# Kernel tuning notes

Hardware: AMD Instinct MI355X
Metric: run time of the kernel (lower is better)

Reference implementation:

```python
import jax, jax.numpy as jnp
import numpy as np

B, T, Hs, Ws, D, NH, NKV = 2, 8, 16, 16, 1024, 16, 4
HD = D // NH  # 64
EPS = 1e-6
THETA = 10000.0


def setup_inputs() -> dict:
    key = jax.random.key(0)
    ks = jax.random.split(key, 6)
    N = T * Hs * Ws
    s = 0.02
    return {
        'x': jax.random.normal(ks[0], (B, N, D), jnp.float32),
        'Wq': jax.random.normal(ks[1], (D, D), jnp.float32) * s,
        'bq': jnp.zeros((D,), jnp.float32),
        'Wk': jax.random.normal(ks[2], (D, NKV * HD), jnp.float32) * s,
        'bk': jnp.zeros((NKV * HD,), jnp.float32),
        'Wv': jax.random.normal(ks[3], (D, NKV * HD), jnp.float32) * s,
        'bv': jnp.zeros((NKV * HD,), jnp.float32),
        'Wo': jax.random.normal(ks[4], (D, D), jnp.float32) * s,
        'bo': jnp.zeros((D,), jnp.float32),
        'qn_w': jnp.ones((HD,), jnp.float32),
        'kn_w': jnp.ones((HD,), jnp.float32),
        't': T, 'h': Hs, 'w': Ws,
    }


def _rms_norm(x, w):
    # RMSNorm over last dim (head_dim), eps=1e-6, learned scale
    var = jnp.mean(jnp.square(x), axis=-1, keepdims=True)
    return x * jax.lax.rsqrt(var + EPS) * w


def _rope_cs(n, d):
    inv = 1.0 / (THETA ** (np.arange(0, d, 2, dtype=np.float32) / d))
    fr = np.arange(n, dtype=np.float32)[:, None] * inv[None, :]
    emb = np.concatenate([fr, fr], axis=-1)  # (n, d)
    return jnp.asarray(np.cos(emb)), jnp.asarray(np.sin(emb))


def _rot_half(x):
    x1, x2 = jnp.split(x, 2, axis=-1)
    return jnp.concatenate([-x2, x1], axis=-1)


def _st_rope(x, t, h, w):
    # x: (B, t, h, w, heads, hd); factored 3D RoPE on head_dim split
    d = x.shape[-1]
    if d % 3 == 0:
        dt = dh = d // 3
        dw = d - 2 * dt
    else:
        dt = d // 4
        dh = d // 4
        dw = d - dt - dh
    xt, xh, xw = jnp.split(x, [dt, dt + dh], axis=-1)

    def app(xs, n, axis_pos, dd):
        cos, sin = _rope_cs(n, dd)
        shp = [1] * 6
        shp[axis_pos] = n
        shp[-1] = dd
        cos = cos.reshape(shp)
        sin = sin.reshape(shp)
        return xs * cos + _rot_half(xs) * sin

    xt = app(xt, t, 1, dt)
    xh = app(xh, h, 2, dh)
    xw = app(xw, w, 3, dw)
    return jnp.concatenate([xt, xh, xw], axis=-1)


def reference(x, Wq, bq, Wk, bk, Wv, bv, Wo, bo, qn_w, kn_w, t, h, w):
    Bx, N, Dx = x.shape
    q = (x @ Wq + bq).reshape(Bx, N, NH, HD)
    k = (x @ Wk + bk).reshape(Bx, N, NKV, HD)
    v = (x @ Wv + bv).reshape(Bx, N, NKV, HD)
    q = _rms_norm(q, qn_w)
    k = _rms_norm(k, kn_w)
    q = _st_rope(q.reshape(Bx, t, h, w, NH, HD), t, h, w).reshape(Bx, N, NH, HD)
    k = _st_rope(k.reshape(Bx, t, h, w, NKV, HD), t, h, w).reshape(Bx, N, NKV, HD)
    g = NH // NKV
    if g > 1:  # GQA: 'b m h d -> b m (h g) d'
        k = jnp.repeat(k, g, axis=2)
        v = jnp.repeat(v, g, axis=2)
    scale = HD ** -0.5
    scores = jnp.einsum('bnhd,bmhd->bhnm', q, k) * scale  # (B,H,N,N)
    p = jax.nn.softmax(scores, axis=-1)
    out = jnp.einsum('bhnm,bmhd->bnhd', p, v).reshape(Bx, N, Dx)
    return out @ Wo + bo
```

## Files before the change

### kernel.cpp

```cpp
#include <hip/hip_runtime.h>
#include <hip/hip_bf16.h>
#include <math.h>

constexpr int B_   = 2;
constexpr int N_   = 2048;
constexpr int D_   = 1024;
constexpr int NH_  = 16;
constexpr int NKV_ = 4;
constexpr int HD_  = 64;
constexpr int BN_  = 4096;
constexpr int KVD_ = NKV_ * HD_;
constexpr float EPS_ = 1e-6f;
constexpr float THETA_ = 10000.0f;
constexpr float LOG2E_ = 1.4426950408889634f;

typedef _Float16 half8v __attribute__((ext_vector_type(8)));
typedef _Float16 half4v __attribute__((ext_vector_type(4)));
typedef _Float16 half2v __attribute__((ext_vector_type(2)));
typedef unsigned short ushort8v __attribute__((ext_vector_type(8)));
typedef float f32x4 __attribute__((ext_vector_type(4)));

static __device__ __forceinline__ unsigned short f2h(float f) {
  union { _Float16 h; unsigned short u; } v; v.h = (_Float16)f; return v.u;
}
static __device__ __forceinline__ float h2f(unsigned short u) {
  union { unsigned short u; _Float16 h; } v; v.u = u; return (float)v.h;
}

#if __has_builtin(__builtin_amdgcn_exp2f)
#define EXP2F(x) __builtin_amdgcn_exp2f(x)
#else
#define EXP2F(x) __expf((x) * 0.6931471805599453f)
#endif

static __device__ __forceinline__ void dma16(const unsigned short* g,
                                             unsigned short* l) {
  __builtin_amdgcn_global_load_lds(
      (const __attribute__((address_space(1))) unsigned int*)g,
      (__attribute__((address_space(3))) unsigned int*)l, 16, 0, 0);
}

static __device__ __forceinline__ void wtrans_tile(
    const float* __restrict__ W, int Nw, int K, float scale,
    unsigned short* __restrict__ WTh, unsigned short* __restrict__ WTl,
    int bx, int by, bool lo)
{
  __shared__ float tile[32][33];
  const int k0 = bx * 32, n0 = by * 32;
  const int c = threadIdx.x & 31, rb = threadIdx.x >> 5;
#pragma unroll
  for (int i = 0; i < 4; ++i) {
    const int r = rb + i * 8;
    tile[r][c] = W[(size_t)(k0 + r) * Nw + n0 + c];
  }
  __syncthreads();
#pragma unroll
  for (int i = 0; i < 4; ++i) {
    const int r = rb + i * 8;
    const float v = tile[c][r] * scale;
    const size_t o = (size_t)(n0 + r) * K + k0 + c;
    const unsigned short hi = f2h(v);
    WTh[o] = hi;
    if (lo) WTl[o] = f2h(v - h2f(hi));
  }
}

__global__ __launch_bounds__(256) void prep(
    const float* __restrict__ x,
    const float* __restrict__ Wq, const float* __restrict__ Wk,
    const float* __restrict__ Wv, const float* __restrict__ Wo,
    unsigned short* __restrict__ xh,
    unsigned short* __restrict__ WqT, unsigned short* __restrict__ WkT,
    unsigned short* __restrict__ WvT,
    unsigned short* __restrict__ WoTh, unsigned short* __restrict__ WoTl)
{
  const int bid = blockIdx.x;
  if (bid < 2048) {
    const int i = (bid * 256 + threadIdx.x) * 8;
    const float4 v0 = *(const float4*)(x + i);
    const float4 v1 = *(const float4*)(x + i + 4);
    ushort8v o;
    o[0] = f2h(v0.x); o[1] = f2h(v0.y); o[2] = f2h(v0.z); o[3] = f2h(v0.w);
    o[4] = f2h(v1.x); o[5] = f2h(v1.y); o[6] = f2h(v1.z); o[7] = f2h(v1.w);
    *(ushort8v*)(xh + i) = o;
  } else if (bid < 3072) {
    const int l = bid - 2048;
    wtrans_tile(Wq, D_, D_, 1.0f, WqT, nullptr, l & 31, l >> 5, false);
  } else if (bid < 3328) {
    const int l = bid - 3072;
    wtrans_tile(Wk, KVD_, D_, 1.0f, WkT, nullptr, l & 31, l >> 5, false);
  } else if (bid < 3584) {
    const int l = bid - 3328;
    wtrans_tile(Wv, KVD_, D_, 1.0f, WvT, nullptr, l & 31, l >> 5, false);
  } else {
    const int l = bid - 3584;
    wtrans_tile(Wo, D_, D_, 64.0f, WoTh, WoTl, l & 31, l >> 5, true);
  }
}

__global__ __launch_bounds__(256) void gemm_qkv(
    const unsigned short* __restrict__ xh,
    const unsigned short* __restrict__ WqT, const unsigned short* __restrict__ WkT,
    const unsigned short* __restrict__ WvT,
    const float* __restrict__ bq, const float* __restrict__ bk, const float* __restrict__ bv,
    const float* __restrict__ qn, const float* __restrict__ kn,
    unsigned short* __restrict__ qv, unsigned short* __restrict__ kv,
    unsigned short* __restrict__ vv)
{
  __shared__ unsigned short As[128 * 64];
  __shared__ unsigned short Bs[64 * 64];

  const int y = blockIdx.y;
  const unsigned short* wt; const float* bias; unsigned short* outp; int opitch, col0, mode;
  if (y < 16)      { wt = WqT + (size_t)y * 64 * D_;        bias = bq + y * 64;        outp = qv; opitch = D_;   col0 = y * 64;        mode = 0; }
  else if (y < 20) { wt = WkT + (size_t)(y - 16) * 64 * D_; bias = bk + (y - 16) * 64; outp = kv; opitch = KVD_; col0 = (y - 16) * 64; mode = 1; }
  else             { wt = WvT + (size_t)(y - 20) * 64 * D_; bias = bv + (y - 20) * 64; outp = vv; opitch = KVD_; col0 = (y - 20) * 64; mode = 2; }

  const int bm = blockIdx.x * 128;
  const int tid = threadIdx.x;
  const int w = tid >> 6, lane = tid & 63, quad = lane >> 4, l16 = lane & 15;
  const int lr = lane >> 3;
  const int gc = (lane & 7) ^ lr;
  const int sw = l16 & 7;

  const unsigned short* gA = xh + (size_t)(bm + w * 8 + lr) * D_ + gc * 8;
  const unsigned short* gB = wt + (size_t)(w * 8 + lr) * D_ + gc * 8;

  f32x4 acc[2][4];
#pragma unroll
  for (int i = 0; i < 2; ++i)
#pragma unroll
    for (int j = 0; j < 4; ++j) acc[i][j] = (f32x4){0.f, 0.f, 0.f, 0.f};

  for (int k0 = 0; k0 < D_; k0 += 64) {
    __syncthreads();
#pragma unroll
    for (int rd = 0; rd < 4; ++rd)
      dma16(gA + (size_t)rd * 32 * D_ + k0, &As[rd * 2048 + w * 512]);
#pragma unroll
    for (int rd = 0; rd < 2; ++rd)
      dma16(gB + (size_t)rd * 32 * D_ + k0, &Bs[rd * 2048 + w * 512]);
    __syncthreads();

#pragma unroll
    for (int kk = 0; kk < 2; ++kk) {
      half8v fa[2], fb[4];
#pragma unroll
      for (int mb = 0; mb < 2; ++mb)
        fa[mb] = *(const half8v*)&As[(w * 32 + mb * 16 + l16) * 64 + ((kk * 4 + quad) ^ sw) * 8];
#pragma unroll
      for (int nb = 0; nb < 4; ++nb)
        fb[nb] = *(const half8v*)&Bs[(nb * 16 + l16) * 64 + ((kk * 4 + quad) ^ sw) * 8];
#pragma unroll
      for (int mb = 0; mb < 2; ++mb)
#pragma unroll
        for (int nb = 0; nb < 4; ++nb)
          acc[mb][nb] = __builtin_amdgcn_mfma_f32_16x16x32_f16(fa[mb], fb[nb], acc[mb][nb], 0, 0, 0);
    }
  }

  float bsv[4];
#pragma unroll
  for (int nb = 0; nb < 4; ++nb) bsv[nb] = bias[nb * 16 + l16];

  if (mode == 2) {
#pragma unroll
    for (int mb = 0; mb < 2; ++mb)
#pragma unroll
      for (int nb = 0; nb < 4; ++nb)
#pragma unroll
        for (int r = 0; r < 4; ++r) {
          const int row = bm + w * 32 + mb * 16 + quad * 4 + r;
          outp[(size_t)row * opitch + col0 + nb * 16 + l16] = f2h(acc[mb][nb][r] + bsv[nb]);
        }
    return;
  }

  const float* nwp = (mode == 0) ? qn : kn;
  float wv[4];
#pragma unroll
  for (int nb = 0; nb < 4; ++nb) wv[nb] = nwp[nb * 16 + l16];
  const float f_th = __powf(THETA_, -(float)(l16 & 7) / 8.0f);
  const float f_w  = __powf(THETA_, -(float)l16 / 16.0f);
  const float oscale = (mode == 0) ? 0.125f * LOG2E_ : 1.0f;
  const bool first8 = (l16 & 8) == 0;

  float snw[4], csw[4];
#pragma unroll
  for (int r = 0; r < 4; ++r)
    __sincosf((float)(quad * 4 + r) * f_w, &snw[r], &csw[r]);

#pragma unroll
  for (int mb = 0; mb < 2; ++mb) {
    const int nbase = (bm + w * 32 + mb * 16) & (N_ - 1);
    float snt, cst, snh, csh;
    __sincosf((float)(nbase >> 8) * f_th, &snt, &cst);
    __sincosf((float)((nbase >> 4) & 15) * f_th, &snh, &csh);
#pragma unroll
    for (int r = 0; r < 4; ++r) {
      float v[4];
      float ss = 0.f;
#pragma unroll
      for (int nb = 0; nb < 4; ++nb) { v[nb] = acc[mb][nb][r] + bsv[nb]; ss += v[nb] * v[nb]; }
      ss += __shfl_xor(ss, 1, 64);
      ss += __shfl_xor(ss, 2, 64);
      ss += __shfl_xor(ss, 4, 64);
      ss += __shfl_xor(ss, 8, 64);
      const float rs = rsqrtf(ss * (1.0f / 64.0f) + EPS_);
#pragma unroll
      for (int nb = 0; nb < 4; ++nb) v[nb] *= rs * wv[nb];

      const float p0 = __shfl_xor(v[0], 8, 64);
      const float p1 = __shfl_xor(v[1], 8, 64);
      const float o0 = v[0] * cst + (first8 ? -p0 : p0) * snt;
      const float o1 = v[1] * csh + (first8 ? -p1 : p1) * snh;
      const float o2 = v[2] * csw[r] - v[3] * snw[r];
      const float o3 = v[3] * csw[r] + v[2] * snw[r];

      const int row = bm + w * 32 + mb * 16 + quad * 4 + r;
      const size_t ob = (size_t)row * opitch + col0 + l16;
      outp[ob]      = f2h(o0 * oscale);
      outp[ob + 16] = f2h(o1 * oscale);
      outp[ob + 32] = f2h(o2 * oscale);
      outp[ob + 48] = f2h(o3 * oscale);
    }
  }
}

__global__ __launch_bounds__(256) void gemm_o(
    const unsigned short* __restrict__ ag,
    const unsigned short* __restrict__ WTh, const unsigned short* __restrict__ WTl,
    const float* __restrict__ bo, float* __restrict__ out)
{
  __shared__ unsigned short As[128 * 64];
  __shared__ unsigned short Bh[64 * 64], Bl[64 * 64];

  const int bm = blockIdx.x * 128, bn = blockIdx.y * 64;
  const int tid = threadIdx.x;
  const int w = tid >> 6, lane = tid & 63, quad = lane >> 4, l16 = lane & 15;
  const int lr = lane >> 3;
  const int gc = (lane & 7) ^ lr;
  const int sw = l16 & 7;

  const unsigned short* gA  = ag  + (size_t)(bm + w * 8 + lr) * D_ + gc * 8;
  const unsigned short* gBh = WTh + (size_t)(bn + w * 8 + lr) * D_ + gc * 8;
  const unsigned short* gBl = WTl + (size_t)(bn + w * 8 + lr) * D_ + gc * 8;

  f32x4 acc[2][4];
#pragma unroll
  for (int i = 0; i < 2; ++i)
#pragma unroll
    for (int j = 0; j < 4; ++j) acc[i][j] = (f32x4){0.f, 0.f, 0.f, 0.f};

  for (int k0 = 0; k0 < D_; k0 += 64) {
    __syncthreads();
#pragma unroll
    for (int rd = 0; rd < 4; ++rd)
      dma16(gA + (size_t)rd * 32 * D_ + k0, &As[rd * 2048 + w * 512]);
#pragma unroll
    for (int rd = 0; rd < 2; ++rd) {
      dma16(gBh + (size_t)rd * 32 * D_ + k0, &Bh[rd * 2048 + w * 512]);
      dma16(gBl + (size_t)rd * 32 * D_ + k0, &Bl[rd * 2048 + w * 512]);
    }
    __syncthreads();

#pragma unroll
    for (int kk = 0; kk < 2; ++kk) {
      half8v fa[2], fbh[4], fbl[4];
#pragma unroll
      for (int mb = 0; mb < 2; ++mb)
        fa[mb] = *(const half8v*)&As[(w * 32 + mb * 16 + l16) * 64 + ((kk * 4 + quad) ^ sw) * 8];
#pragma unroll
      for (int nb = 0; nb < 4; ++nb) {
        const int ro = (nb * 16 + l16) * 64 + ((kk * 4 + quad) ^ sw) * 8;
        fbh[nb] = *(const half8v*)&Bh[ro];
        fbl[nb] = *(const half8v*)&Bl[ro];
      }
#pragma unroll
      for (int mb = 0; mb < 2; ++mb)
#pragma unroll
        for (int nb = 0; nb < 4; ++nb) {
          acc[mb][nb] = __builtin_amdgcn_mfma_f32_16x16x32_f16(fa[mb], fbl[nb], acc[mb][nb], 0, 0, 0);
          acc[mb][nb] = __builtin_amdgcn_mfma_f32_16x16x32_f16(fa[mb], fbh[nb], acc[mb][nb], 0, 0, 0);
        }
    }
  }

  float bsv[4];
#pragma unroll
  for (int nb = 0; nb < 4; ++nb) bsv[nb] = bo[bn + nb * 16 + l16];
#pragma unroll
  for (int mb = 0; mb < 2; ++mb)
#pragma unroll
    for (int nb = 0; nb < 4; ++nb)
#pragma unroll
      for (int r = 0; r < 4; ++r) {
        const int row = bm + w * 32 + mb * 16 + quad * 4 + r;
        const int col = bn + nb * 16 + l16;
        out[(size_t)row * D_ + col] = acc[mb][nb][r] * 0.015625f + bsv[nb];
      }
}

__global__ __launch_bounds__(256, 2) void attn_mfma(
    const unsigned short* __restrict__ qg,
    const unsigned short* __restrict__ kg,
    const unsigned short* __restrict__ vg,
    unsigned short* __restrict__ og)
{
  __shared__ unsigned short Ks[2][128 * 64];
  __shared__ unsigned short Vt[2][64][136];

  const int bid = blockIdx.x;
  const int qt  = bid & 15;
  const int h   = (bid >> 4) & 15;
  const int b   = bid >> 8;
  const int kvh = h >> 2;

  const int tid  = threadIdx.x;
  const int w    = tid >> 6;
  const int lane = tid & 63;
  const int quad = lane >> 4;
  const int l16  = lane & 15;
  const int lr = lane >> 3;
  const int gc = (lane & 7) ^ lr;
  const int sw = l16 & 7;

  half8v aq[2][2];
#pragma unroll
  for (int qb = 0; qb < 2; ++qb) {
    const int qrow = qt * 128 + w * 32 + qb * 16 + l16;
    const unsigned short* qptr =
        qg + ((size_t)(b * N_ + qrow) * D_) + h * HD_ + quad * 8;
    aq[qb][0] = *(const half8v*)(qptr);
    aq[qb][1] = *(const half8v*)(qptr + 32);
  }

  f32x4 o_[2][4];
  float lrow[2] = {0.f, 0.f};
#pragma unroll
  for (int qb = 0; qb < 2; ++qb)
#pragma unroll
    for (int i = 0; i < 4; ++i) o_[qb][i] = (f32x4){0.f, 0.f, 0.f, 0.f};

  const unsigned short* gK =
      kg + ((size_t)(b * N_) + w * 8 + lr) * KVD_ + kvh * HD_ + gc * 8;

  const int vj = tid & 15;
  const int vh = (tid >> 4) & 1;
  const int vs = (tid >> 5) & 7;
  const int vcol = vh * 32 + ((vj >> 1) & 3) * 8 + ((vj >> 3) & 1) * 4 + 2 * (vj & 1);
  const unsigned short* gV =
      vg + (size_t)(b * N_ + 2 * vj + 32 * vh) * KVD_ + kvh * HD_ + 8 * vs;

#pragma unroll
  for (int rd = 0; rd < 4; ++rd)
    dma16(gK + (size_t)(rd * 32) * KVD_, &Ks[0][rd * 2048 + w * 512]);
  ushort8v va[2][2];
#pragma unroll
  for (int hh = 0; hh < 2; ++hh) {
    const unsigned short* p = gV + (size_t)(hh * 64) * KVD_;
    va[hh][0] = *(const ushort8v*)(p);
    va[hh][1] = *(const ushort8v*)(p + KVD_);
  }
#pragma unroll
  for (int hh = 0; hh < 2; ++hh)
#pragma unroll
    for (int i = 0; i < 8; ++i)
      *(unsigned int*)&Vt[0][8 * vs + i][hh * 64 + vcol] =
          (unsigned int)va[hh][0][i] | ((unsigned int)va[hh][1][i] << 16);
#pragma unroll
  for (int hh = 0; hh < 2; ++hh) {
    const unsigned short* p = gV + (size_t)(128 + hh * 64) * KVD_;
    va[hh][0] = *(const ushort8v*)(p);
    va[hh][1] = *(const ushort8v*)(p + KVD_);
  }
  __syncthreads();

  for (int kt = 0; kt < 16; ++kt) {
    const int cur = kt & 1;
    if (kt < 15) {
#pragma unroll
      for (int rd = 0; rd < 4; ++rd)
        dma16(gK + (size_t)((kt + 1) * 128 + rd * 32) * KVD_,
              &Ks[cur ^ 1][rd * 2048 + w * 512]);
#pragma unroll
      for (int hh = 0; hh < 2; ++hh)
#pragma unroll
        for (int i = 0; i < 8; ++i)
          *(unsigned int*)&Vt[cur ^ 1][8 * vs + i][hh * 64 + vcol] =
              (unsigned int)va[hh][0][i] | ((unsigned int)va[hh][1][i] << 16);
      if (kt < 14) {
#pragma unroll
        for (int hh = 0; hh < 2; ++hh) {
          const unsigned short* p = gV + (size_t)((kt + 2) * 128 + hh * 64) * KVD_;
          va[hh][0] = *(const ushort8v*)(p);
          va[hh][1] = *(const ushort8v*)(p + KVD_);
        }
      }
    }

#pragma unroll
    for (int hh = 0; hh < 2; ++hh) {
      f32x4 s[2][4];
#pragma unroll
      for (int nb = 0; nb < 4; ++nb) {
        const int kr = (hh * 64 + nb * 16 + l16) * 64;
        const half8v b0 = *(const half8v*)&Ks[cur][kr + (quad ^ sw) * 8];
        const half8v b1 = *(const half8v*)&Ks[cur][kr + ((4 + quad) ^ sw) * 8];
#pragma unroll
        for (int qb = 0; qb < 2; ++qb) {
          f32x4 z = (f32x4){0.f, 0.f, 0.f, 0.f};
          z = __builtin_amdgcn_mfma_f32_16x16x32_f16(b0, aq[qb][0], z, 0, 0, 0);
          s[qb][nb] = __builtin_amdgcn_mfma_f32_16x16x32_f16(b1, aq[qb][1], z, 0, 0, 0);
        }
      }

      half8v pf[2][2];
#pragma unroll
      for (int qb = 0; qb < 2; ++qb) {
        float ls = 0.f;
#pragma unroll
        for (int nb = 0; nb < 4; ++nb) {
          const float p0 = EXP2F(s[qb][nb][0]);
          const float p1 = EXP2F(s[qb][nb][1]);
          const float p2 = EXP2F(s[qb][nb][2]);
          const float p3 = EXP2F(s[qb][nb][3]);
          ls += (p0 + p1) + (p2 + p3);
          const int kc = nb >> 1, jo = (nb & 1) * 4;
          pf[qb][kc][jo + 0] = (_Float16)p0;
          pf[qb][kc][jo + 1] = (_Float16)p1;
          pf[qb][kc][jo + 2] = (_Float16)p2;
          pf[qb][kc][jo + 3] = (_Float16)p3;
        }
        lrow[qb] += ls;
      }

#pragma unroll
      for (int kc = 0; kc < 2; ++kc)
#pragma unroll
        for (int nb = 0; nb < 4; ++nb) {
          const half8v bv =
              *(const half8v*)&Vt[cur][nb * 16 + l16][hh * 64 + kc * 32 + quad * 8];
#pragma unroll
          for (int qb = 0; qb < 2; ++qb)
            o_[qb][nb] = __builtin_amdgcn_mfma_f32_16x16x32_f16(bv, pf[qb][kc], o_[qb][nb], 0, 0, 0);
        }
    }
    __syncthreads();
  }

#pragma unroll
  for (int qb = 0; qb < 2; ++qb) {
    float l = lrow[qb];
    l += __shfl_xor(l, 16, 64);
    l += __shfl_xor(l, 32, 64);
    const float inv = 1.0f / l;
    const int qrow = qt * 128 + w * 32 + qb * 16 + l16;
    const size_t base = (size_t)(b * N_ + qrow) * D_ + h * HD_;
#pragma unroll
    for (int nb = 0; nb < 4; ++nb) {
      half4v pk;
#pragma unroll
      for (int r = 0; r < 4; ++r) pk[r] = (_Float16)(o_[qb][nb][r] * inv);
      *(half4v*)&og[base + nb * 16 + quad * 4] = pk;
    }
  }
}

extern "C" void kernel_launch(void* const* d_in, const int* in_sizes, int n_in,
                              void* d_out, int out_size, void* d_ws, size_t ws_size,
                              hipStream_t stream) {
  const float* x  = (const float*)d_in[0];
  const float* Wq = (const float*)d_in[1];
  const float* bq = (const float*)d_in[2];
  const float* Wk = (const float*)d_in[3];
  const float* bk = (const float*)d_in[4];
  const float* Wv = (const float*)d_in[5];
  const float* bv = (const float*)d_in[6];
  const float* Wo = (const float*)d_in[7];
  const float* bo = (const float*)d_in[8];
  const float* qn = (const float*)d_in[9];
  const float* kn = (const float*)d_in[10];
  float* out = (float*)d_out;

  const size_t M4 = (size_t)BN_ * D_;
  const size_t M1 = (size_t)BN_ * KVD_;
  unsigned short* xh  = (unsigned short*)d_ws;
  unsigned short* qv  = xh + M4;
  unsigned short* kv  = qv + M4;
  unsigned short* vv  = kv + M1;
  unsigned short* WqT = vv + M1;
  unsigned short* WkT = WqT + (size_t)D_ * D_;
  unsigned short* WvT = WkT + (size_t)D_ * KVD_;
  unsigned short* WoTh = WvT + (size_t)D_ * KVD_;
  unsigned short* WoTl = WoTh + (size_t)D_ * D_;
  unsigned short* og  = xh;

  const dim3 blk(256);

  prep<<<dim3(4608), blk, 0, stream>>>(x, Wq, Wk, Wv, Wo, xh, WqT, WkT, WvT, WoTh, WoTl);

  gemm_qkv<<<dim3(32, 24), blk, 0, stream>>>(xh, WqT, WkT, WvT, bq, bk, bv, qn, kn, qv, kv, vv);

  attn_mfma<<<dim3(B_ * NH_ * (N_ / 128)), blk, 0, stream>>>(qv, kv, vv, og);

  gemm_o<<<dim3(32, 16), blk, 0, stream>>>(og, WoTh, WoTl, bo, out);
}
```

Measured before the change: 179.3 us.

## Enlarge attention blocks to 256 query rows with 8 waves sharing K/V tiles

The attention kernel now runs 512-thread blocks covering 256 query rows each, so every K/V tile staged in shared memory serves twice as many queries. The K DMA and V transpose loads are split across the larger thread group, so each thread does half the staging work. This halves global K/V traffic and the number of blocks, but gives fewer blocks (256) for the GPU's CUs and makes each synchronization span eight waves. Launch bounds rise to 512 threads with a minimum of 4 blocks, which may tighten register limits.

```diff
diff --git a/kernel.cpp b/kernel.cpp
--- a/kernel.cpp
+++ b/kernel.cpp
@@ -301,7 +301,7 @@
       }
 }
 
-__global__ __launch_bounds__(256, 2) void attn_mfma(
+__global__ __launch_bounds__(512, 4) void attn_mfma(
     const unsigned short* __restrict__ qg,
     const unsigned short* __restrict__ kg,
     const unsigned short* __restrict__ vg,
@@ -311,9 +311,9 @@
   __shared__ unsigned short Vt[2][64][136];
 
   const int bid = blockIdx.x;
-  const int qt  = bid & 15;
-  const int h   = (bid >> 4) & 15;
-  const int b   = bid >> 8;
+  const int qt  = bid & 7;
+  const int h   = (bid >> 3) & 15;
+  const int b   = bid >> 7;
   const int kvh = h >> 2;
 
   const int tid  = threadIdx.x;
@@ -328,7 +328,7 @@
   half8v aq[2][2];
 #pragma unroll
   for (int qb = 0; qb < 2; ++qb) {
-    const int qrow = qt * 128 + w * 32 + qb * 16 + l16;
+    const int qrow = qt * 256 + w * 32 + qb * 16 + l16;
     const unsigned short* qptr =
         qg + ((size_t)(b * N_ + qrow) * D_) + h * HD_ + quad * 8;
     aq[qb][0] = *(const half8v*)(qptr);
@@ -345,34 +345,28 @@
   const unsigned short* gK =
       kg + ((size_t)(b * N_) + w * 8 + lr) * KVD_ + kvh * HD_ + gc * 8;
 
-  const int vj = tid & 15;
-  const int vh = (tid >> 4) & 1;
-  const int vs = (tid >> 5) & 7;
-  const int vcol = vh * 32 + ((vj >> 1) & 3) * 8 + ((vj >> 3) & 1) * 4 + 2 * (vj & 1);
+  const int vj  = tid & 15;
+  const int vh  = (tid >> 4) & 1;
+  const int vs  = (tid >> 5) & 7;
+  const int vhh = tid >> 8;
+  const int vcol = vhh * 64 + vh * 32 +
+                   ((vj >> 1) & 3) * 8 + ((vj >> 3) & 1) * 4 + 2 * (vj & 1);
   const unsigned short* gV =
-      vg + (size_t)(b * N_ + 2 * vj + 32 * vh) * KVD_ + kvh * HD_ + 8 * vs;
-
-#pragma unroll
-  for (int rd = 0; rd < 4; ++rd)
-    dma16(gK + (size_t)(rd * 32) * KVD_, &Ks[0][rd * 2048 + w * 512]);
-  ushort8v va[2][2];
-#pragma unroll
-  for (int hh = 0; hh < 2; ++hh) {
-    const unsigned short* p = gV + (size_t)(hh * 64) * KVD_;
-    va[hh][0] = *(const ushort8v*)(p);
-    va[hh][1] = *(const ushort8v*)(p + KVD_);
-  }
-#pragma unroll
-  for (int hh = 0; hh < 2; ++hh)
-#pragma unroll
-    for (int i = 0; i < 8; ++i)
-      *(unsigned int*)&Vt[0][8 * vs + i][hh * 64 + vcol] =
-          (unsigned int)va[hh][0][i] | ((unsigned int)va[hh][1][i] << 16);
-#pragma unroll
-  for (int hh = 0; hh < 2; ++hh) {
-    const unsigned short* p = gV + (size_t)(128 + hh * 64) * KVD_;
-    va[hh][0] = *(const ushort8v*)(p);
-    va[hh][1] = *(const ushort8v*)(p + KVD_);
+      vg + (size_t)(b * N_ + vhh * 64 + 2 * vj + 32 * vh) * KVD_ + kvh * HD_ + 8 * vs;
+
+#pragma unroll
+  for (int rd = 0; rd < 2; ++rd)
+    dma16(gK + (size_t)(rd * 64) * KVD_, &Ks[0][rd * 4096 + w * 512]);
+  ushort8v va0 = *(const ushort8v*)(gV);
+  ushort8v va1 = *(const ushort8v*)(gV + KVD_);
+#pragma unroll
+  for (int i = 0; i < 8; ++i)
+    *(unsigned int*)&Vt[0][8 * vs + i][vcol] =
+        (unsigned int)va0[i] | ((unsigned int)va1[i] << 16);
+  {
+    const unsigned short* p = gV + (size_t)128 * KVD_;
+    va0 = *(const ushort8v*)(p);
+    va1 = *(const ushort8v*)(p + KVD_);
   }
   __syncthreads();
 
@@ -380,22 +374,17 @@
     const int cur = kt & 1;
     if (kt < 15) {
 #pragma unroll
-      for (int rd = 0; rd < 4; ++rd)
-        dma16(gK + (size_t)((kt + 1) * 128 + rd * 32) * KVD_,
-              &Ks[cur ^ 1][rd * 2048 + w * 512]);
-#pragma unroll
-      for (int hh = 0; hh < 2; ++hh)
-#pragma unroll
-        for (int i = 0; i < 8; ++i)
-          *(unsigned int*)&Vt[cur ^ 1][8 * vs + i][hh * 64 + vcol] =
-              (unsigned int)va[hh][0][i] | ((unsigned int)va[hh][1][i] << 16);
+      for (int rd = 0; rd < 2; ++rd)
+        dma16(gK + (size_t)((kt + 1) * 128 + rd * 64) * KVD_,
+              &Ks[cur ^ 1][rd * 4096 + w * 512]);
+#pragma unroll
+      for (int i = 0; i < 8; ++i)
+        *(unsigned int*)&Vt[cur ^ 1][8 * vs + i][vcol] =
+            (unsigned int)va0[i] | ((unsigned int)va1[i] << 16);
       if (kt < 14) {
-#pragma unroll
-        for (int hh = 0; hh < 2; ++hh) {
-          const unsigned short* p = gV + (size_t)((kt + 2) * 128 + hh * 64) * KVD_;
-          va[hh][0] = *(const ushort8v*)(p);
-          va[hh][1] = *(const ushort8v*)(p + KVD_);
-        }
+        const unsigned short* p = gV + (size_t)(kt + 2) * 128 * KVD_;
+        va0 = *(const ushort8v*)(p);
+        va1 = *(const ushort8v*)(p + KVD_);
       }
     }
 
@@ -455,7 +444,7 @@
     l += __shfl_xor(l, 16, 64);
     l += __shfl_xor(l, 32, 64);
     const float inv = 1.0f / l;
-    const int qrow = qt * 128 + w * 32 + qb * 16 + l16;
+    const int qrow = qt * 256 + w * 32 + qb * 16 + l16;
     const size_t base = (size_t)(b * N_ + qrow) * D_ + h * HD_;
 #pragma unroll
     for (int nb = 0; nb < 4; ++nb) {
@@ -502,7 +491,7 @@
 
   gemm_qkv<<<dim3(32, 24), blk, 0, stream>>>(xh, WqT, WkT, WvT, bq, bk, bv, qn, kn, qv, kv, vv);
 
-  attn_mfma<<<dim3(B_ * NH_ * (N_ / 128)), blk, 0, stream>>>(qv, kv, vv, og);
+  attn_mfma<<<dim3(B_ * NH_ * (N_ / 256)), dim3(512), 0, stream>>>(qv, kv, vv, og);
 
   gemm_o<<<dim3(32, 16), blk, 0, stream>>>(og, WoTh, WoTl, bo, out);
 }
```

New measurement: 225.8 us. 1.26x slower.
